# Kernel optimization log

Hardware: AMD Instinct MI355X
Metric: run time of the kernel (lower is better)

## Reference

```python
import jax, jax.numpy as jnp
import numpy as np

DIM, H, HD = 1024, 16, 64
B, S = 2, 2048
LAMBDA_INIT = 0.8


def _mha(x, wq, bq, wk, bk, wv, bv, wo, bo):
    # x: [B,S,DIM]; wq/wk/wv: [DIM,H,HD]; wo: [H,HD,DIM]
    q = jnp.einsum('btd,dhk->bthk', x, wq) + bq
    k = jnp.einsum('bsd,dhk->bshk', x, wk) + bk
    v = jnp.einsum('bsd,dhk->bshk', x, wv) + bv
    scores = jnp.einsum('bthk,bshk->bhts', q, k) / jnp.sqrt(jnp.asarray(HD, x.dtype))
    attn = jax.nn.softmax(scores, axis=-1)
    out = jnp.einsum('bhts,bshk->bthk', attn, v)
    return jnp.einsum('bthk,hkd->btd', out, wo) + bo


def _get_lambda(lambda_param, layer_idx):
    layer_factor = jnp.clip(jnp.asarray(layer_idx, jnp.float32) * 0.3, 0.0, 5.0)
    offset = 0.6 * jnp.exp(-layer_factor)
    lam = jax.nn.sigmoid(lambda_param) * (1.0 - offset) + 0.2
    return jnp.clip(lam, 0.1, 0.9)


def setup_inputs() -> dict:
    key = jax.random.key(0)
    ks = jax.random.split(key, 10)
    sc_in = 1.0 / np.sqrt(DIM)   # fan-in-ish scale for projections
    sc_out = 1.0 / np.sqrt(H * HD)
    d = {
        'x': jax.random.normal(ks[0], (B, S, DIM), jnp.float32),
        'proj_w': jax.random.normal(ks[1], (DIM, DIM), jnp.float32) * sc_in,
        'proj_b': jnp.zeros((DIM,), jnp.float32),
        'lambda_param': jnp.full((1,), np.log(LAMBDA_INIT) - np.log(1.0 - LAMBDA_INIT), jnp.float32),
        'layer_idx': 0,
    }
    for i, kk in zip((1, 2), (ks[2:6], ks[6:10])):
        d[f'wq{i}'] = jax.random.normal(kk[0], (DIM, H, HD), jnp.float32) * sc_in
        d[f'wk{i}'] = jax.random.normal(kk[1], (DIM, H, HD), jnp.float32) * sc_in
        d[f'wv{i}'] = jax.random.normal(kk[2], (DIM, H, HD), jnp.float32) * sc_in
        d[f'wo{i}'] = jax.random.normal(kk[3], (H, HD, DIM), jnp.float32) * sc_out
        d[f'bq{i}'] = jnp.zeros((H, HD), jnp.float32)
        d[f'bk{i}'] = jnp.zeros((H, HD), jnp.float32)
        d[f'bv{i}'] = jnp.zeros((H, HD), jnp.float32)
        d[f'bo{i}'] = jnp.zeros((DIM,), jnp.float32)
    return d


def reference(x, wq1, bq1, wk1, bk1, wv1, bv1, wo1, bo1,
              wq2, bq2, wk2, bk2, wv2, bv2, wo2, bo2,
              proj_w, proj_b, lambda_param, layer_idx):
    out1 = _mha(x, wq1, bq1, wk1, bk1, wv1, bv1, wo1, bo1)
    out2 = _mha(x, wq2, bq2, wk2, bk2, wv2, bv2, wo2, bo2)
    lam = _get_lambda(lambda_param, layer_idx)  # shape (1,)
    y = (1.0 - lam) * out1 + lam * out2
    return jnp.einsum('btd,de->bte', y, proj_w) + proj_b
```

## Files before the change

kernel.cpp:

```cpp
#include <hip/hip_runtime.h>

#define DEVI __device__ __forceinline__

typedef unsigned short u16;
typedef unsigned int u32;
typedef __bf16 bf16x8 __attribute__((ext_vector_type(8)));
typedef float f32x4 __attribute__((ext_vector_type(4)));
typedef float f32x16 __attribute__((ext_vector_type(16)));

#define SCALE_Q 0.1803368801f

typedef const __attribute__((address_space(1))) void cas1_void;
typedef __attribute__((address_space(3))) void as3_void;

DEVI void lds_dma16(const void* g, void* l) {
  __builtin_amdgcn_global_load_lds((cas1_void*)g, (as3_void*)l, 16, 0, 0);
}

DEVI u16 f2bf(float f) {
  union { float f; u32 u; } v; v.f = f;
  u32 r = v.u + 0x7FFFu + ((v.u >> 16) & 1u);
  return (u16)(r >> 16);
}

DEVI float exp2n(float x) {
#if __has_builtin(__builtin_amdgcn_exp2f)
  return __builtin_amdgcn_exp2f(x);
#else
  return __expf(x * 0.6931471805599453f);
#endif
}

DEVI u32 pk2(float lo, float hi2) {
  union { __bf16 h[2]; u32 u; } p;
  p.h[0] = (__bf16)lo; p.h[1] = (__bf16)hi2;
  return p.u;
}

DEVI float lambda_dev(const float* lamp, const int* lidx) {
  float lf = (float)(*lidx) * 0.3f;
  lf = fminf(fmaxf(lf, 0.0f), 5.0f);
  float offset = 0.6f * expf(-lf);
  float s = 1.0f / (1.0f + expf(-lamp[0]));
  float lam = s * (1.0f - offset) + 0.2f;
  return fminf(fmaxf(lam, 0.1f), 0.9f);
}

__global__ __launch_bounds__(256) void k_cvt(const float* __restrict__ x, u16* __restrict__ o) {
  int i = (blockIdx.x * 256 + threadIdx.x) * 8;
  float4 a = *(const float4*)(x + i);
  float4 b = *(const float4*)(x + i + 4);
  union { u16 s[8]; uint4 v; } r;
  r.s[0] = f2bf(a.x); r.s[1] = f2bf(a.y); r.s[2] = f2bf(a.z); r.s[3] = f2bf(a.w);
  r.s[4] = f2bf(b.x); r.s[5] = f2bf(b.y); r.s[6] = f2bf(b.z); r.s[7] = f2bf(b.w);
  *(uint4*)(o + i) = r.v;
}

struct TransArgs {
  const float* src[9];
  u16* dst[9];
  int dld[9];
  int dcol[9];
  int smode[9];
};

__global__ __launch_bounds__(256) void k_transpose(TransArgs ta, const float* lamp, const int* lidx) {
  __shared__ float tile[32][33];
  int z = blockIdx.z;
  int tx = threadIdx.x & 31, ty = threadIdx.x >> 5;
  int bx = blockIdx.x * 32, by = blockIdx.y * 32;
  const float* s = ta.src[z];
#pragma unroll
  for (int i = 0; i < 4; ++i)
    tile[ty + i * 8][tx] = s[(size_t)(by + ty + i * 8) * 1024 + bx + tx];
  __syncthreads();
  float sc = 1.0f;
  int m = ta.smode[z];
  if (m == 1) sc = SCALE_Q;
  else if (m >= 2) {
    float lam = lambda_dev(lamp, lidx);
    sc = (m == 2) ? (1.0f - lam) : lam;
  }
  u16* d = ta.dst[z];
  size_t ld = (size_t)ta.dld[z];
#pragma unroll
  for (int i = 0; i < 4; ++i) {
    int dr = bx + ty + i * 8;
    d[(size_t)dr * ld + ta.dcol[z] + by + tx] = f2bf(sc * tile[tx][ty + i * 8]);
  }
}

struct GemmArgs {
  const u16* A;
  const u16* Bt[6];
  const float* bias0[6];
  float bscale[6];
  u16* dstu[6];
  const float* bias1;
  float* dstf;
  const float* lamp;
  const int* lidx;
  int K;
  int mode;
};

__global__ __launch_bounds__(256) void k_gemm(GemmArgs ga) {
  __shared__ __align__(16) u16 smem[32768];
  char* smc = (char*)smem;
  const int t = threadIdx.x;
  const int lane = t & 63;
  const int l15 = lane & 15, hi = lane >> 4;
  const int w = t >> 6, wm = w >> 1, wn = w & 1;
  const int m0 = blockIdx.y * 128, n0 = blockIdx.x * 128;
  const int z = (ga.mode == 0) ? (int)blockIdx.z : 0;
  const u16* A = ga.A;
  const u16* Bt = ga.Bt[z];
  const int K = ga.K;

  const char* gA[4];
  const char* gB[4];
  u32 lof[4];
#pragma unroll
  for (int ii = 0; ii < 4; ++ii) {
    int fl = ii * 256 + t;
    int row = fl >> 3;
    int cb = ((fl & 7) * 16) ^ ((row & 7) << 4);
    gA[ii] = (const char*)(A + (size_t)(m0 + row) * K) + cb;
    gB[ii] = (const char*)(Bt + (size_t)(n0 + row) * K) + cb;
    lof[ii] = (u32)(ii * 256 + (t & ~63)) * 16;
  }

  u32 aoff[4], boff[4];
#pragma unroll
  for (int i = 0; i < 4; ++i) {
    int rA = wm * 64 + i * 16 + l15;
    aoff[i] = (u32)rA * 128 + (u32)((hi * 16) ^ ((rA & 7) << 4));
    int rB = wn * 64 + i * 16 + l15;
    boff[i] = 16384u + (u32)rB * 128 + (u32)((hi * 16) ^ ((rB & 7) << 4));
  }

  const f32x4 fz = {0.f, 0.f, 0.f, 0.f};
  f32x4 acc[4][4];
#pragma unroll
  for (int i = 0; i < 4; ++i)
#pragma unroll
    for (int j = 0; j < 4; ++j) acc[i][j] = fz;

  const int NT = K >> 6;
#pragma unroll
  for (int ii = 0; ii < 4; ++ii) {
    lds_dma16(gA[ii], smc + lof[ii]);
    lds_dma16(gB[ii], smc + 16384 + lof[ii]);
  }
  __syncthreads();
  int cur = 0;
  for (int kt = 0; kt < NT; ++kt) {
    if (kt + 1 < NT) {
      const u32 nb = (u32)(cur ^ 1) * 32768u;
      size_t soff = (size_t)(kt + 1) * 128;
#pragma unroll
      for (int ii = 0; ii < 4; ++ii) {
        lds_dma16(gA[ii] + soff, smc + nb + lof[ii]);
        lds_dma16(gB[ii] + soff, smc + nb + 16384 + lof[ii]);
      }
    }
    const u32 bb = (u32)cur * 32768u;
#pragma unroll
    for (int kh = 0; kh < 2; ++kh) {
      const u32 kx = (u32)kh << 6;
      bf16x8 af[4], bfr[4];
#pragma unroll
      for (int i = 0; i < 4; ++i) af[i] = *(const bf16x8*)(smc + bb + (aoff[i] ^ kx));
#pragma unroll
      for (int j = 0; j < 4; ++j) bfr[j] = *(const bf16x8*)(smc + bb + (boff[j] ^ kx));
#pragma unroll
      for (int i = 0; i < 4; ++i)
#pragma unroll
        for (int j = 0; j < 4; ++j)
          acc[i][j] = __builtin_amdgcn_mfma_f32_16x16x32_bf16(af[i], bfr[j], acc[i][j], 0, 0, 0);
    }
    __syncthreads();
    cur ^= 1;
  }

  const int mode = ga.mode;
  float lam = 0.f;
  if (mode == 1) lam = lambda_dev(ga.lamp, ga.lidx);
  const float* b0 = ga.bias0[z];
  const float bsc = ga.bscale[z];
  const int kind = z % 3;
  u16* du = ga.dstu[z];

#pragma unroll
  for (int i = 0; i < 4; ++i) {
#pragma unroll
    for (int j = 0; j < 4; ++j) {
#pragma unroll
      for (int jj = 0; jj < 4; ++jj) {
        int m = m0 + wm * 64 + i * 16 + hi * 4 + jj;
        int n = n0 + wn * 64 + j * 16 + l15;
        float v = acc[i][j][jj];
        if (mode == 0) {
          v += b0[n] * bsc;
          int b = m >> 11, s = m & 2047, h = n >> 6, hd = n & 63;
          size_t addr;
          if (kind != 2) addr = ((size_t)(b * 16 + h) * 2048 + s) * 64 + hd;
          else           addr = ((size_t)(b * 16 + h) * 64 + hd) * 2048 + s;
          du[addr] = f2bf(v);
        } else if (mode == 1) {
          v += (1.0f - lam) * b0[n] + lam * ga.bias1[n];
          du[(size_t)m * 1024 + n] = f2bf(v);
        } else {
          v += b0[n];
          ga.dstf[(size_t)m * 1024 + n] = v;
        }
      }
    }
  }
}

DEVI void stage64(const char* gbase, int gstride, char* lbase, int t) {
#pragma unroll
  for (int it = 0; it < 2; ++it) {
    int flat = it * 256 + t;
    int row = flat >> 3;
    int col = (flat & 7) * 16;
    lds_dma16(gbase + (size_t)row * gstride + (col ^ ((row & 7) << 4)),
              lbase + (size_t)(it * 256 + (t & ~63)) * 16);
  }
}

__global__ __launch_bounds__(256, 3) void k_attn2(const u16* __restrict__ Qg_, const u16* __restrict__ Kg_,
                                                  const u16* __restrict__ Vg_, u16* __restrict__ AO) {
  __shared__ __align__(16) u16 Ksm[2][4096];
  __shared__ __align__(16) u16 Vsm[2][4096];
  const int t = threadIdx.x, lane = t & 63, w = t >> 6;
  const int l31 = lane & 31, hi = lane >> 5;
  const int bid = blockIdx.x;
  const int xcd = bid & 7, slot = bid >> 3;
  const int qt = slot & 15;
  const int bhbr = xcd * 8 + (slot >> 4);
  const int br = bhbr >> 5, bh = bhbr & 31;
  const size_t base = ((size_t)br * 32 + bh) * (size_t)(2048 * 64);
  const u16* Qg = Qg_ + base;
  const char* Kgc = (const char*)(Kg_ + base);
  const char* Vgc = (const char*)(Vg_ + base);
  const int q0 = qt * 128 + w * 32;

  bf16x8 qf[4];
  {
    const u16* qp = Qg + (size_t)(q0 + l31) * 64 + hi * 8;
#pragma unroll
    for (int ks = 0; ks < 4; ++ks) qf[ks] = *(const bf16x8*)(qp + ks * 16);
  }

  f32x16 accO[2];
#pragma unroll
  for (int b = 0; b < 2; ++b)
#pragma unroll
    for (int r = 0; r < 16; ++r) accO[b][r] = 0.f;
  float l_r = 0.f;

  stage64(Kgc, 128, (char*)Ksm[0], t);
  stage64(Vgc, 4096, (char*)Vsm[0], t);
  __syncthreads();

  for (int kvt = 0; kvt < 32; ++kvt) {
    const int cur = kvt & 1;
    if (kvt < 31) {
      const int kv0n = (kvt + 1) * 64;
      stage64(Kgc + (size_t)kv0n * 128, 128, (char*)Ksm[cur ^ 1], t);
      stage64(Vgc + (size_t)kv0n * 2, 4096, (char*)Vsm[cur ^ 1], t);
    }
    const char* Kb = (const char*)Ksm[cur];
    const char* Vb = (const char*)Vsm[cur];

    f32x16 st[2];
#pragma unroll
    for (int kvs = 0; kvs < 2; ++kvs)
#pragma unroll
      for (int r = 0; r < 16; ++r) st[kvs][r] = 0.f;
#pragma unroll
    for (int kvs = 0; kvs < 2; ++kvs) {
      const int row = l31 + 32 * kvs;
      const int sw = (row & 7) << 4;
#pragma unroll
      for (int ks = 0; ks < 4; ++ks) {
        bf16x8 kf = *(const bf16x8*)(Kb + row * 128 + ((ks * 32 + hi * 16) ^ sw));
        st[kvs] = __builtin_amdgcn_mfma_f32_32x32x16_bf16(kf, qf[ks], st[kvs], 0, 0, 0);
      }
    }

    float sum = 0.f;
#pragma unroll
    for (int kvs = 0; kvs < 2; ++kvs)
#pragma unroll
      for (int r = 0; r < 16; ++r) {
        const float p = exp2n(st[kvs][r]);
        st[kvs][r] = p;
        sum += p;
      }
    sum += __shfl_xor(sum, 32);
    l_r += sum;

    bf16x8 pa[4];
#pragma unroll
    for (int kvs = 0; kvs < 2; ++kvs)
#pragma unroll
      for (int half = 0; half < 2; ++half) {
        const int rb = half * 8;
        u32 a0 = pk2(st[kvs][rb + 0], st[kvs][rb + 1]);
        u32 a1 = pk2(st[kvs][rb + 2], st[kvs][rb + 3]);
        u32 b0 = pk2(st[kvs][rb + 4], st[kvs][rb + 5]);
        u32 b1 = pk2(st[kvs][rb + 6], st[kvs][rb + 7]);
        u32 ta0 = __shfl_xor(a0, 32), ta1 = __shfl_xor(a1, 32);
        u32 tb0 = __shfl_xor(b0, 32), tb1 = __shfl_xor(b1, 32);
        union { u32 u[4]; bf16x8 v; } pk;
        pk.u[0] = hi ? tb0 : a0;
        pk.u[1] = hi ? tb1 : a1;
        pk.u[2] = hi ? b0 : ta0;
        pk.u[3] = hi ? b1 : ta1;
        pa[kvs * 2 + half] = pk.v;
      }

#pragma unroll
    for (int hs = 0; hs < 2; ++hs) {
      const int row = l31 + 32 * hs;
      const int sw = (row & 7) << 4;
#pragma unroll
      for (int ks = 0; ks < 4; ++ks) {
        bf16x8 vf = *(const bf16x8*)(Vb + row * 128 + ((ks * 32 + hi * 16) ^ sw));
        accO[hs] = __builtin_amdgcn_mfma_f32_32x32x16_bf16(pa[ks], vf, accO[hs], 0, 0, 0);
      }
    }
    __syncthreads();
  }

  const int b = bh >> 4, h = bh & 15;
  const float inv = 1.0f / l_r;
#pragma unroll
  for (int r = 0; r < 16; ++r) {
    const int qr = (r & 3) + 8 * (r >> 2) + 4 * hi;
    const float iv = __shfl(inv, qr);
    const size_t mrow = (size_t)(b * 2048 + q0 + qr);
#pragma unroll
    for (int hs = 0; hs < 2; ++hs) {
      const int col = br * 1024 + h * 64 + hs * 32 + l31;
      AO[mrow * 2048 + col] = f2bf(accO[hs][r] * iv);
    }
  }
}

extern "C" void kernel_launch(void* const* d_in, const int* in_sizes, int n_in,
                              void* d_out, int out_size, void* d_ws, size_t ws_size,
                              hipStream_t stream) {
  (void)in_sizes; (void)n_in; (void)out_size; (void)ws_size;
  const float* x      = (const float*)d_in[0];
  const float* proj_w = (const float*)d_in[1];
  const float* proj_b = (const float*)d_in[2];
  const float* lamp   = (const float*)d_in[3];
  const int*   lidx   = (const int*)d_in[4];
  const float* wq1 = (const float*)d_in[5];
  const float* wk1 = (const float*)d_in[6];
  const float* wv1 = (const float*)d_in[7];
  const float* wo1 = (const float*)d_in[8];
  const float* bq1 = (const float*)d_in[9];
  const float* bk1 = (const float*)d_in[10];
  const float* bv1 = (const float*)d_in[11];
  const float* bo1 = (const float*)d_in[12];
  const float* wq2 = (const float*)d_in[13];
  const float* wk2 = (const float*)d_in[14];
  const float* wv2 = (const float*)d_in[15];
  const float* wo2 = (const float*)d_in[16];
  const float* bq2 = (const float*)d_in[17];
  const float* bk2 = (const float*)d_in[18];
  const float* bv2 = (const float*)d_in[19];
  const float* bo2 = (const float*)d_in[20];

  char* ws = (char*)d_ws;
  const size_t MB = 1024 * 1024;
  u16* xb  = (u16*)(ws);
  u16* Wt  = (u16*)(ws + 8 * MB);
  u16* WOt = (u16*)(ws + 20 * MB);
  u16* PWt = (u16*)(ws + 24 * MB);
  u16* Qb  = (u16*)(ws + 26 * MB);
  u16* Kb  = (u16*)(ws + 42 * MB);
  u16* Vb  = (u16*)(ws + 58 * MB);
  u16* AOb = (u16*)(ws);
  u16* yb  = (u16*)(ws + 26 * MB);

  k_cvt<<<2048, 256, 0, stream>>>(x, xb);

  TransArgs ta;
  const float* srcs[9] = {wq1, wk1, wv1, wq2, wk2, wv2, wo1, wo2, proj_w};
  u16* dsts[9] = {Wt, Wt + 1048576, Wt + 2097152, Wt + 3145728, Wt + 4194304, Wt + 5242880,
                  WOt, WOt, PWt};
  int dld[9]   = {1024, 1024, 1024, 1024, 1024, 1024, 2048, 2048, 1024};
  int dcol[9]  = {0, 0, 0, 0, 0, 0, 0, 1024, 0};
  int smode[9] = {1, 0, 0, 1, 0, 0, 2, 3, 0};
  for (int i = 0; i < 9; ++i) {
    ta.src[i] = srcs[i]; ta.dst[i] = dsts[i]; ta.dld[i] = dld[i];
    ta.dcol[i] = dcol[i]; ta.smode[i] = smode[i];
  }
  k_transpose<<<dim3(32, 32, 9), 256, 0, stream>>>(ta, lamp, lidx);

  GemmArgs g0 = {};
  g0.A = xb; g0.K = 1024; g0.mode = 0;
  const float* qkvb[6] = {bq1, bk1, bv1, bq2, bk2, bv2};
  const size_t BRS = 4194304;
  u16* qkvd[6] = {Qb, Kb, Vb, Qb + BRS, Kb + BRS, Vb + BRS};
  float bsc[6] = {SCALE_Q, 1.f, 1.f, SCALE_Q, 1.f, 1.f};
  for (int i = 0; i < 6; ++i) {
    g0.Bt[i] = Wt + (size_t)i * 1048576;
    g0.bias0[i] = qkvb[i];
    g0.bscale[i] = bsc[i];
    g0.dstu[i] = qkvd[i];
  }
  k_gemm<<<dim3(8, 32, 6), 256, 0, stream>>>(g0);

  k_attn2<<<1024, 256, 0, stream>>>(Qb, Kb, Vb, AOb);

  GemmArgs g1 = {};
  g1.A = AOb; g1.K = 2048; g1.mode = 1;
  g1.Bt[0] = WOt; g1.bias0[0] = bo1; g1.bscale[0] = 1.f;
  g1.bias1 = bo2; g1.dstu[0] = yb; g1.lamp = lamp; g1.lidx = lidx;
  k_gemm<<<dim3(8, 32, 1), 256, 0, stream>>>(g1);

  GemmArgs g2 = {};
  g2.A = yb; g2.K = 1024; g2.mode = 2;
  g2.Bt[0] = PWt; g2.bias0[0] = proj_b; g2.bscale[0] = 1.f;
  g2.dstf = (float*)d_out;
  k_gemm<<<dim3(8, 32, 1), 256, 0, stream>>>(g2);
}
```

Measured before the change: 290.2 us.

## Pre-swizzle K/V into MFMA fragment order and load directly into registers

The QKV GEMM epilogue now writes K and V in a fragment-major layout that matches the MFMA operand order. The attention kernel drops LDS staging and block barriers, and each wave loads its K/V fragments straight from global memory into registers, prefetching the next tile during compute. This removes LDS traffic and __syncthreads, at the cost of every wave reading K/V separately from global/L2 (4x redundant per block). It also uses more registers, so launch bounds drop to 2 blocks per CU.

```diff
diff --git a/kernel.cpp b/kernel.cpp
--- a/kernel.cpp
+++ b/kernel.cpp
@@ -204,8 +204,15 @@
           v += b0[n] * bsc;
           int b = m >> 11, s = m & 2047, h = n >> 6, hd = n & 63;
           size_t addr;
-          if (kind != 2) addr = ((size_t)(b * 16 + h) * 2048 + s) * 64 + hd;
-          else           addr = ((size_t)(b * 16 + h) * 64 + hd) * 2048 + s;
+          if (kind == 0) {
+            addr = ((size_t)(b * 16 + h) * 2048 + s) * 64 + hd;
+          } else if (kind == 1) {
+            int gf = ((s >> 5) * 8 + (hd >> 4) * 2 + ((hd >> 3) & 1)) * 32 + (s & 31);
+            addr = ((size_t)(b * 16 + h) * 16384 + gf) * 8 + (hd & 7);
+          } else {
+            int gf = ((((s >> 6) * 4 + ((s >> 4) & 3)) * 2 + ((s >> 3) & 1)) * 2 + (hd >> 5)) * 32 + (hd & 31);
+            addr = ((size_t)(b * 16 + h) * 16384 + gf) * 8 + (s & 7);
+          }
           du[addr] = f2bf(v);
         } else if (mode == 1) {
           v += (1.0f - lam) * b0[n] + lam * ga.bias1[n];
@@ -219,21 +226,8 @@
   }
 }
 
-DEVI void stage64(const char* gbase, int gstride, char* lbase, int t) {
-#pragma unroll
-  for (int it = 0; it < 2; ++it) {
-    int flat = it * 256 + t;
-    int row = flat >> 3;
-    int col = (flat & 7) * 16;
-    lds_dma16(gbase + (size_t)row * gstride + (col ^ ((row & 7) << 4)),
-              lbase + (size_t)(it * 256 + (t & ~63)) * 16);
-  }
-}
-
-__global__ __launch_bounds__(256, 3) void k_attn2(const u16* __restrict__ Qg_, const u16* __restrict__ Kg_,
+__global__ __launch_bounds__(256, 2) void k_attn3(const u16* __restrict__ Qg_, const u16* __restrict__ Kg_,
                                                   const u16* __restrict__ Vg_, u16* __restrict__ AO) {
-  __shared__ __align__(16) u16 Ksm[2][4096];
-  __shared__ __align__(16) u16 Vsm[2][4096];
   const int t = threadIdx.x, lane = t & 63, w = t >> 6;
   const int l31 = lane & 31, hi = lane >> 5;
   const int bid = blockIdx.x;
@@ -241,10 +235,10 @@
   const int qt = slot & 15;
   const int bhbr = xcd * 8 + (slot >> 4);
   const int br = bhbr >> 5, bh = bhbr & 31;
-  const size_t base = ((size_t)br * 32 + bh) * (size_t)(2048 * 64);
+  const size_t base = ((size_t)br * 32 + bh) * 131072;
   const u16* Qg = Qg_ + base;
-  const char* Kgc = (const char*)(Kg_ + base);
-  const char* Vgc = (const char*)(Vg_ + base);
+  const u16* Kt = Kg_ + base + (size_t)(hi * 256 + l31 * 8);
+  const u16* Vt = Vg_ + base + (size_t)(hi * 512 + l31 * 8);
   const int q0 = qt * 128 + w * 32;
 
   bf16x8 qf[4];
@@ -261,34 +255,36 @@
     for (int r = 0; r < 16; ++r) accO[b][r] = 0.f;
   float l_r = 0.f;
 
-  stage64(Kgc, 128, (char*)Ksm[0], t);
-  stage64(Vgc, 4096, (char*)Vsm[0], t);
-  __syncthreads();
+  bf16x8 kf[2][4], vf[2][4];
+#pragma unroll
+  for (int kvs = 0; kvs < 2; ++kvs)
+#pragma unroll
+    for (int ks = 0; ks < 4; ++ks)
+      kf[kvs][ks] = *(const bf16x8*)(Kt + kvs * 2048 + ks * 512);
+#pragma unroll
+  for (int hs = 0; hs < 2; ++hs)
+#pragma unroll
+    for (int ks = 0; ks < 4; ++ks)
+      vf[hs][ks] = *(const bf16x8*)(Vt + ks * 1024 + hs * 256);
 
   for (int kvt = 0; kvt < 32; ++kvt) {
-    const int cur = kvt & 1;
+    f32x16 st[2];
+#pragma unroll
+    for (int kvs = 0; kvs < 2; ++kvs)
+#pragma unroll
+      for (int r = 0; r < 16; ++r) st[kvs][r] = 0.f;
+#pragma unroll
+    for (int ks = 0; ks < 4; ++ks) {
+      st[0] = __builtin_amdgcn_mfma_f32_32x32x16_bf16(kf[0][ks], qf[ks], st[0], 0, 0, 0);
+      st[1] = __builtin_amdgcn_mfma_f32_32x32x16_bf16(kf[1][ks], qf[ks], st[1], 0, 0, 0);
+    }
     if (kvt < 31) {
-      const int kv0n = (kvt + 1) * 64;
-      stage64(Kgc + (size_t)kv0n * 128, 128, (char*)Ksm[cur ^ 1], t);
-      stage64(Vgc + (size_t)kv0n * 2, 4096, (char*)Vsm[cur ^ 1], t);
-    }
-    const char* Kb = (const char*)Ksm[cur];
-    const char* Vb = (const char*)Vsm[cur];
-
-    f32x16 st[2];
-#pragma unroll
-    for (int kvs = 0; kvs < 2; ++kvs)
-#pragma unroll
-      for (int r = 0; r < 16; ++r) st[kvs][r] = 0.f;
-#pragma unroll
-    for (int kvs = 0; kvs < 2; ++kvs) {
-      const int row = l31 + 32 * kvs;
-      const int sw = (row & 7) << 4;
-#pragma unroll
-      for (int ks = 0; ks < 4; ++ks) {
-        bf16x8 kf = *(const bf16x8*)(Kb + row * 128 + ((ks * 32 + hi * 16) ^ sw));
-        st[kvs] = __builtin_amdgcn_mfma_f32_32x32x16_bf16(kf, qf[ks], st[kvs], 0, 0, 0);
-      }
+      const u16* kp = Kt + (size_t)(kvt + 1) * 4096;
+#pragma unroll
+      for (int kvs = 0; kvs < 2; ++kvs)
+#pragma unroll
+        for (int ks = 0; ks < 4; ++ks)
+          kf[kvs][ks] = *(const bf16x8*)(kp + kvs * 2048 + ks * 512);
     }
 
     float sum = 0.f;
@@ -324,16 +320,18 @@
       }
 
 #pragma unroll
-    for (int hs = 0; hs < 2; ++hs) {
-      const int row = l31 + 32 * hs;
-      const int sw = (row & 7) << 4;
-#pragma unroll
-      for (int ks = 0; ks < 4; ++ks) {
-        bf16x8 vf = *(const bf16x8*)(Vb + row * 128 + ((ks * 32 + hi * 16) ^ sw));
-        accO[hs] = __builtin_amdgcn_mfma_f32_32x32x16_bf16(pa[ks], vf, accO[hs], 0, 0, 0);
-      }
-    }
-    __syncthreads();
+    for (int ks = 0; ks < 4; ++ks) {
+      accO[0] = __builtin_amdgcn_mfma_f32_32x32x16_bf16(pa[ks], vf[0][ks], accO[0], 0, 0, 0);
+      accO[1] = __builtin_amdgcn_mfma_f32_32x32x16_bf16(pa[ks], vf[1][ks], accO[1], 0, 0, 0);
+    }
+    if (kvt < 31) {
+      const u16* vp = Vt + (size_t)(kvt + 1) * 4096;
+#pragma unroll
+      for (int hs = 0; hs < 2; ++hs)
+#pragma unroll
+        for (int ks = 0; ks < 4; ++ks)
+          vf[hs][ks] = *(const bf16x8*)(vp + ks * 1024 + hs * 256);
+    }
   }
 
   const int b = bh >> 4, h = bh & 15;
@@ -418,7 +416,7 @@
   }
   k_gemm<<<dim3(8, 32, 6), 256, 0, stream>>>(g0);
 
-  k_attn2<<<1024, 256, 0, stream>>>(Qb, Kb, Vb, AOb);
+  k_attn3<<<1024, 256, 0, stream>>>(Qb, Kb, Vb, AOb);
 
   GemmArgs g1 = {};
   g1.A = AOb; g1.K = 2048; g1.mode = 1;
```

New measurement: 275.6 us. 5.0% less time.
